# Optimization experiments

Hardware: AMD Instinct MI355X
Metric: run time of the kernel (lower is better)

Reference implementation:

```python
import jax, jax.numpy as jnp
import numpy as np

BATCH = 65536
FEAT_DIM = 512
NUM_CLASS = 16
LAMDA = 1.0
LAMDA1 = 10.0
SCALE = 1.0
EPS = 1e-9


def setup_inputs() -> dict:
    key = jax.random.key(0)
    k1, k2, k3 = jax.random.split(key, 3)
    output_features = jax.random.normal(k1, (BATCH, FEAT_DIM), dtype=jnp.float32)
    y_truth = jax.random.randint(k2, (BATCH,), 0, NUM_CLASS, dtype=jnp.int64)
    feature_centers = jax.random.normal(k3, (NUM_CLASS, FEAT_DIM), dtype=jnp.float32)
    return {
        "output_features": output_features,
        "y_truth": y_truth,
        "feature_centers": feature_centers,
    }


def reference(output_features, y_truth, feature_centers):
    batch_size = output_features.shape[0]
    factor = SCALE / batch_size

    # Center loss: gather per-sample class center, squared diff, sum.
    centers_batch = feature_centers[y_truth]              # [B, D]
    diff = output_features - centers_batch
    loss_center = 0.5 * jnp.sum(diff * diff) * factor

    # Pairwise cosine similarity over class centers (upper triangle, j<k),
    # replacing the O(C^2) python loop with one matmul + mask + reduce.
    norms = jnp.sqrt(jnp.sum(feature_centers * feature_centers, axis=1))  # [C]
    gram = feature_centers @ feature_centers.T                            # [C, C]
    denom = norms[:, None] * norms[None, :] + EPS
    cos = gram / denom
    c = feature_centers.shape[0]
    upper = jnp.triu(jnp.ones((c, c), dtype=bool), k=1)
    item1_sum = jnp.sum(jnp.where(upper, cos + 1.0, 0.0))

    loss_island = LAMDA * (loss_center + LAMDA1 * item1_sum)
    return loss_island
```

## Files before the change

kernel.cpp:

```cpp
#include <hip/hip_runtime.h>
#include <math.h>

#define BATCH    65536
#define FEAT     512
#define NCLASS   16
#define LAMDA    1.0f
#define LAMDA1   10.0f
#define SCALE    1.0f
#define EPS      1e-9f

constexpr int BLOCK  = 256;
constexpr int GRID   = 4096;
constexpr int NV     = BATCH * (FEAT / 4);
constexpr int STRIDE = GRID * BLOCK;
constexpr int ITERS  = NV / STRIDE;

typedef float f4v __attribute__((ext_vector_type(4)));

__global__ __launch_bounds__(BLOCK) void center_loss_kernel(
    const f4v* __restrict__ x,
    const int* __restrict__ y,
    const f4v* __restrict__ centers4,
    float*     __restrict__ partials)
{
    const int tid = blockIdx.x * BLOCK + threadIdx.x;

    const int base_b = __builtin_amdgcn_readfirstlane(tid >> 7);
    const int d4     = tid & 127;

    int cls[ITERS];
    #pragma unroll
    for (int it = 0; it < ITERS; ++it)
        cls[it] = y[base_b + it * (STRIDE >> 7)];

    float sum = 0.0f;
    #pragma unroll
    for (int it = 0; it < ITERS; ++it) {
        f4v xv = __builtin_nontemporal_load(&x[tid + it * STRIDE]);
        f4v cv = centers4[cls[it] * (FEAT / 4) + d4];
        f4v e  = xv - cv;
        sum += e.x * e.x + e.y * e.y + e.z * e.z + e.w * e.w;
    }

    #pragma unroll
    for (int off = 32; off > 0; off >>= 1)
        sum += __shfl_down(sum, off, 64);

    __shared__ float wsum[4];
    const int lane = threadIdx.x & 63;
    const int wid  = threadIdx.x >> 6;
    if (lane == 0) wsum[wid] = sum;
    __syncthreads();
    if (threadIdx.x == 0) {
        partials[blockIdx.x] = wsum[0] + wsum[1] + wsum[2] + wsum[3];
    }
}

__global__ __launch_bounds__(256) void finalize_kernel(
    const f4v*   __restrict__ centers4,
    const float* __restrict__ partials,
    float*       __restrict__ out)
{
    float psum = 0.0f;
    #pragma unroll
    for (int k = 0; k < GRID / 256; ++k)
        psum += partials[threadIdx.x + k * 256];
    #pragma unroll
    for (int off = 32; off > 0; off >>= 1)
        psum += __shfl_down(psum, off, 64);

    __shared__ float wsum[4];
    const int lane = threadIdx.x & 63;
    const int wid  = threadIdx.x >> 6;
    if (lane == 0) wsum[wid] = psum;

    __shared__ float gram[NCLASS][NCLASS];
    const int j = threadIdx.x >> 4;
    const int k = threadIdx.x & 15;
    const f4v* cj = centers4 + j * (FEAT / 4);
    const f4v* ck = centers4 + k * (FEAT / 4);
    float dot = 0.0f;
    #pragma unroll 8
    for (int i = 0; i < FEAT / 4; ++i) {
        f4v a = cj[i];
        f4v b = ck[i];
        dot += a.x * b.x + a.y * b.y + a.z * b.z + a.w * b.w;
    }
    gram[j][k] = dot;
    __syncthreads();

    if (threadIdx.x == 0) {
        float item1 = 0.0f;
        for (int jj = 0; jj < NCLASS; ++jj) {
            float nj = sqrtf(gram[jj][jj]);
            for (int kk = jj + 1; kk < NCLASS; ++kk) {
                float nk = sqrtf(gram[kk][kk]);
                item1 += gram[jj][kk] / (nj * nk + EPS) + 1.0f;
            }
        }
        float total = wsum[0] + wsum[1] + wsum[2] + wsum[3];
        float loss_center = 0.5f * total * (SCALE / (float)BATCH);
        out[0] = LAMDA * (loss_center + LAMDA1 * item1);
    }
}

extern "C" void kernel_launch(void* const* d_in, const int* in_sizes, int n_in,
                              void* d_out, int out_size, void* d_ws, size_t ws_size,
                              hipStream_t stream) {
    const float* x       = (const float*)d_in[0];
    const int*   y       = (const int*)d_in[1];
    const float* centers = (const float*)d_in[2];
    float* out      = (float*)d_out;
    float* partials = (float*)d_ws;

    center_loss_kernel<<<GRID, BLOCK, 0, stream>>>(
        (const f4v*)x, y, (const f4v*)centers, partials);

    finalize_kernel<<<1, 256, 0, stream>>>((const f4v*)centers, partials, out);
}
```

Before: 207.2 us.

## Fuse center-loss and finalize kernels with last-block atomic reduction

Merges the two kernels into one launch: an extra block computes the Gram matrix into workspace, and the last block to increment an atomic counter does the final partial-sum reduction and cosine term. It also issues all x loads before the center gathers so more memory requests are in flight. This removes the second kernel launch and its dependency gap, but adds a hipMemsetAsync to reset the counter, plus threadfence and atomic overhead in every block.

```diff
diff --git a/kernel.cpp b/kernel.cpp
--- a/kernel.cpp
+++ b/kernel.cpp
@@ -15,92 +15,111 @@
 constexpr int STRIDE = GRID * BLOCK;
 constexpr int ITERS  = NV / STRIDE;
 
+constexpr int WS_GRAM = GRID;
+constexpr int WS_CTR  = GRID + NCLASS * NCLASS;
+
 typedef float f4v __attribute__((ext_vector_type(4)));
 
-__global__ __launch_bounds__(BLOCK) void center_loss_kernel(
+__global__ __launch_bounds__(BLOCK) void island_fused(
     const f4v* __restrict__ x,
     const int* __restrict__ y,
     const f4v* __restrict__ centers4,
-    float*     __restrict__ partials)
+    float*     __restrict__ ws,
+    float*     __restrict__ out)
 {
-    const int tid = blockIdx.x * BLOCK + threadIdx.x;
+    __shared__ float wsum[4];
+    __shared__ int   slast;
 
-    const int base_b = __builtin_amdgcn_readfirstlane(tid >> 7);
-    const int d4     = tid & 127;
+    float*        partials = ws;
+    float*        gramws   = ws + WS_GRAM;
+    unsigned int* ctr      = (unsigned int*)(ws + WS_CTR);
 
-    int cls[ITERS];
-    #pragma unroll
-    for (int it = 0; it < ITERS; ++it)
-        cls[it] = y[base_b + it * (STRIDE >> 7)];
+    const int bid  = blockIdx.x;
+    const int lane = threadIdx.x & 63;
+    const int wid  = threadIdx.x >> 6;
 
-    float sum = 0.0f;
-    #pragma unroll
-    for (int it = 0; it < ITERS; ++it) {
-        f4v xv = __builtin_nontemporal_load(&x[tid + it * STRIDE]);
-        f4v cv = centers4[cls[it] * (FEAT / 4) + d4];
-        f4v e  = xv - cv;
-        sum += e.x * e.x + e.y * e.y + e.z * e.z + e.w * e.w;
+    if (bid < GRID) {
+        const int tid = bid * BLOCK + threadIdx.x;
+
+        const int base_b = __builtin_amdgcn_readfirstlane(tid >> 7);
+        const int d4     = tid & 127;
+
+        int cls[ITERS];
+        #pragma unroll
+        for (int it = 0; it < ITERS; ++it)
+            cls[it] = y[base_b + it * (STRIDE >> 7)];
+
+        f4v xv[ITERS];
+        #pragma unroll
+        for (int it = 0; it < ITERS; ++it)
+            xv[it] = __builtin_nontemporal_load(&x[tid + it * STRIDE]);
+
+        float sum = 0.0f;
+        #pragma unroll
+        for (int it = 0; it < ITERS; ++it) {
+            f4v cv = centers4[cls[it] * (FEAT / 4) + d4];
+            f4v e  = xv[it] - cv;
+            sum += e.x * e.x + e.y * e.y + e.z * e.z + e.w * e.w;
+        }
+
+        #pragma unroll
+        for (int off = 32; off > 0; off >>= 1)
+            sum += __shfl_down(sum, off, 64);
+
+        if (lane == 0) wsum[wid] = sum;
+        __syncthreads();
+        if (threadIdx.x == 0)
+            partials[bid] = wsum[0] + wsum[1] + wsum[2] + wsum[3];
+    } else {
+        const int j = threadIdx.x >> 4;
+        const int k = threadIdx.x & 15;
+        const f4v* cj = centers4 + j * (FEAT / 4);
+        const f4v* ck = centers4 + k * (FEAT / 4);
+        float dot = 0.0f;
+        #pragma unroll 8
+        for (int i = 0; i < FEAT / 4; ++i) {
+            f4v a = cj[i];
+            f4v b = ck[i];
+            dot += a.x * b.x + a.y * b.y + a.z * b.z + a.w * b.w;
+        }
+        gramws[threadIdx.x] = dot;
+        __syncthreads();
     }
 
-    #pragma unroll
-    for (int off = 32; off > 0; off >>= 1)
-        sum += __shfl_down(sum, off, 64);
-
-    __shared__ float wsum[4];
-    const int lane = threadIdx.x & 63;
-    const int wid  = threadIdx.x >> 6;
-    if (lane == 0) wsum[wid] = sum;
-    __syncthreads();
     if (threadIdx.x == 0) {
-        partials[blockIdx.x] = wsum[0] + wsum[1] + wsum[2] + wsum[3];
+        __threadfence();
+        unsigned int old = atomicAdd(ctr, 1u);
+        slast = (old == (unsigned int)GRID) ? 1 : 0;
     }
-}
-
-__global__ __launch_bounds__(256) void finalize_kernel(
-    const f4v*   __restrict__ centers4,
-    const float* __restrict__ partials,
-    float*       __restrict__ out)
-{
-    float psum = 0.0f;
-    #pragma unroll
-    for (int k = 0; k < GRID / 256; ++k)
-        psum += partials[threadIdx.x + k * 256];
-    #pragma unroll
-    for (int off = 32; off > 0; off >>= 1)
-        psum += __shfl_down(psum, off, 64);
-
-    __shared__ float wsum[4];
-    const int lane = threadIdx.x & 63;
-    const int wid  = threadIdx.x >> 6;
-    if (lane == 0) wsum[wid] = psum;
-
-    __shared__ float gram[NCLASS][NCLASS];
-    const int j = threadIdx.x >> 4;
-    const int k = threadIdx.x & 15;
-    const f4v* cj = centers4 + j * (FEAT / 4);
-    const f4v* ck = centers4 + k * (FEAT / 4);
-    float dot = 0.0f;
-    #pragma unroll 8
-    for (int i = 0; i < FEAT / 4; ++i) {
-        f4v a = cj[i];
-        f4v b = ck[i];
-        dot += a.x * b.x + a.y * b.y + a.z * b.z + a.w * b.w;
-    }
-    gram[j][k] = dot;
     __syncthreads();
 
-    if (threadIdx.x == 0) {
-        float item1 = 0.0f;
-        for (int jj = 0; jj < NCLASS; ++jj) {
-            float nj = sqrtf(gram[jj][jj]);
-            for (int kk = jj + 1; kk < NCLASS; ++kk) {
-                float nk = sqrtf(gram[kk][kk]);
-                item1 += gram[jj][kk] / (nj * nk + EPS) + 1.0f;
+    if (slast) {
+        __threadfence();
+
+        float psum = 0.0f;
+        #pragma unroll
+        for (int k2 = 0; k2 < GRID / 256; ++k2)
+            psum += partials[threadIdx.x + k2 * 256];
+        #pragma unroll
+        for (int off = 32; off > 0; off >>= 1)
+            psum += __shfl_down(psum, off, 64);
+
+        if (lane == 0) wsum[wid] = psum;
+        __syncthreads();
+
+        if (threadIdx.x == 0) {
+            float item1 = 0.0f;
+            for (int jj = 0; jj < NCLASS; ++jj) {
+                float nj = sqrtf(gramws[jj * NCLASS + jj]);
+                for (int kk = jj + 1; kk < NCLASS; ++kk) {
+                    float nk = sqrtf(gramws[kk * NCLASS + kk]);
+                    item1 += gramws[jj * NCLASS + kk] / (nj * nk + EPS) + 1.0f;
+                }
             }
+            float total = wsum[0] + wsum[1] + wsum[2] + wsum[3];
+            float loss_center = 0.5f * total * (SCALE / (float)BATCH);
+            out[0] = LAMDA * (loss_center + LAMDA1 * item1);
         }
-        float total = wsum[0] + wsum[1] + wsum[2] + wsum[3];
-        float loss_center = 0.5f * total * (SCALE / (float)BATCH);
-        out[0] = LAMDA * (loss_center + LAMDA1 * item1);
     }
 }
 
@@ -110,11 +129,12 @@
     const float* x       = (const float*)d_in[0];
     const int*   y       = (const int*)d_in[1];
     const float* centers = (const float*)d_in[2];
-    float* out      = (float*)d_out;
-    float* partials = (float*)d_ws;
+    float* out = (float*)d_out;
+    float* ws  = (float*)d_ws;
 
-    center_loss_kernel<<<GRID, BLOCK, 0, stream>>>(
-        (const f4v*)x, y, (const f4v*)centers, partials);
+    hipMemsetAsync((char*)d_ws + (size_t)WS_CTR * sizeof(float), 0,
+                   sizeof(unsigned int), stream);
 
-    finalize_kernel<<<1, 256, 0, stream>>>((const f4v*)centers, partials, out);
+    island_fused<<<GRID + 1, BLOCK, 0, stream>>>(
+        (const f4v*)x, y, (const f4v*)centers, ws, out);
 }
```

New measurement: 406.0 us. 1.96x slower.
